# Kernel tuning notes

Hardware: AMD Instinct MI355X
Metric: run time of the kernel (lower is better)

## Reference

```python
import jax, jax.numpy as jnp
import numpy as np

B, T, C, H, D = 8, 1, 4096, 32, 128
P, PS = 32, 128  # num pages, page size


def setup_inputs() -> dict:
    key = jax.random.key(0)
    ks = jax.random.split(key, 8)
    w = 0.02  # weight init scale
    return {
        "x": jax.random.normal(ks[0], (B, T, C), jnp.float32),
        "k_pages": jax.random.normal(ks[1], (P, B, H, PS, D), jnp.float32),
        "v_pages": jax.random.normal(ks[2], (P, B, H, PS, D), jnp.float32),
        "Wq": jax.random.normal(ks[3], (C, C), jnp.float32) * w,
        "bq": jnp.zeros((C,), jnp.float32),
        "Wk": jax.random.normal(ks[4], (C, C), jnp.float32) * w,
        "bk": jnp.zeros((C,), jnp.float32),
        "Wv": jax.random.normal(ks[5], (C, C), jnp.float32) * w,
        "bv": jnp.zeros((C,), jnp.float32),
        "Wo": jax.random.normal(ks[6], (C, C), jnp.float32) * w,
        "bo": jnp.zeros((C,), jnp.float32),
        "cur_pos": 4095,  # tokens already in cache before this step
    }


def reference(x, k_pages, v_pages, Wq, bq, Wk, bk, Wv, bv, Wo, bo, cur_pos):
    b, t, c = x.shape
    scale = 1.0 / float(np.sqrt(D))

    def proj(W, bias):
        # [B,T,C] -> [B,H,T,D]
        y = x @ W.T + bias
        return y.reshape(b, t, H, D).transpose(0, 2, 1, 3)

    q = proj(Wq, bq)
    k_new = proj(Wk, bk)
    v_new = proj(Wv, bv)

    # kv_cache.update(k, v): write the T new tokens at cur_pos (static int)
    page, off = cur_pos // PS, cur_pos % PS
    k_pages = k_pages.at[page, :, :, off:off + t, :].set(k_new)
    v_pages = v_pages.at[page, :, :, off:off + t, :].set(v_new)

    # After update cur_pos + T == P*PS, so every page is fully valid.
    # Online-softmax over pages == exact softmax over the concatenated cache.
    k_all = k_pages.transpose(1, 2, 0, 3, 4).reshape(b, H, P * PS, D)
    v_all = v_pages.transpose(1, 2, 0, 3, 4).reshape(b, H, P * PS, D)

    scores = jnp.einsum("bhtd,bhsd->bhts", q, k_all) * scale
    attn = jax.nn.softmax(scores, axis=-1)
    out = jnp.einsum("bhts,bhsd->bhtd", attn, v_all)
    out = out.transpose(0, 2, 1, 3).reshape(b, t, c)
    return out @ Wo.T + bo
```

## Files before the change

kernel.cpp:

```cpp
#include <hip/hip_runtime.h>
#include <math.h>

#define Bn 8
#define Hn 32
#define Dn 128
#define Cn 4096
#define PSn 128
#define NCHUNK 16
#define CHUNK 256

extern "C" __global__ __launch_bounds__(256) void gemv8(
    const float* __restrict__ xin,
    const float* __restrict__ W0, const float* __restrict__ b0,
    const float* __restrict__ W1, const float* __restrict__ b1,
    const float* __restrict__ W2, const float* __restrict__ b2,
    float* __restrict__ ybase)
{
    const int m    = blockIdx.y;
    const float* W    = (m == 0) ? W0 : ((m == 1) ? W1 : W2);
    const float* bias = (m == 0) ? b0 : ((m == 1) ? b1 : b2);
    float* y = ybase + (size_t)m * (Bn * Cn);

    const int wv   = threadIdx.x >> 6;
    const int lane = threadIdx.x & 63;
    const int obase = blockIdx.x * 8;

    float acc[8][8];
#pragma unroll
    for (int r = 0; r < 8; ++r)
#pragma unroll
        for (int j = 0; j < 8; ++j) acc[r][j] = 0.f;

    const float* wp = W + (size_t)obase * Cn;
#pragma unroll
    for (int it = 0; it < 4; ++it) {
        const int c = wv * 1024 + it * 256 + lane * 4;
        float4 w4[8], x4[8];
#pragma unroll
        for (int j = 0; j < 8; ++j) w4[j] = *(const float4*)(wp + (size_t)j * Cn + c);
#pragma unroll
        for (int r = 0; r < 8; ++r) x4[r] = *(const float4*)(xin + (size_t)r * Cn + c);
#pragma unroll
        for (int r = 0; r < 8; ++r)
#pragma unroll
            for (int j = 0; j < 8; ++j) {
                acc[r][j] = fmaf(x4[r].x, w4[j].x,
                            fmaf(x4[r].y, w4[j].y,
                            fmaf(x4[r].z, w4[j].z,
                            fmaf(x4[r].w, w4[j].w, acc[r][j]))));
            }
    }

    const int lr = lane >> 3, lj = lane & 7;
    float mine = 0.f;
#pragma unroll
    for (int r = 0; r < 8; ++r)
#pragma unroll
        for (int j = 0; j < 8; ++j) {
            float v = acc[r][j];
#pragma unroll
            for (int off = 32; off; off >>= 1) v += __shfl_xor(v, off);
            if (lr == r && lj == j) mine = v;
        }

    __shared__ float red[4][64];
    red[wv][lane] = mine;
    __syncthreads();
    if (threadIdx.x < 64) {
        const float s = red[0][lane] + red[1][lane] + red[2][lane] + red[3][lane]
                      + bias[obase + lj];
        y[(size_t)lr * Cn + obase + lj] = s;
    }
}

extern "C" __global__ __launch_bounds__(256) void attn_partial(
    const float* __restrict__ kp, const float* __restrict__ vp,
    const float* __restrict__ qn, const float* __restrict__ kn,
    const float* __restrict__ vn, const int* __restrict__ curp,
    float* __restrict__ pout, float* __restrict__ pml)
{
    const int chunk = blockIdx.x, h = blockIdx.y, b = blockIdx.z;
    const int tid = threadIdx.x;
    const int cur = *curp;

    __shared__ float  sc[CHUNK];
    __shared__ float  wred[8];
    __shared__ float4 red[8][32];

    const int l32 = tid & 31;
    const int g   = tid >> 5;
    const float4 q4   = *(const float4*)(qn + (size_t)b * Cn + h * Dn + l32 * 4);
    const float* newk = kn + (size_t)b * Cn + h * Dn;
    const float* newv = vn + (size_t)b * Cn + h * Dn;
    const int s0 = chunk * CHUNK;
    const float* kbase = kp + (((size_t)b * Hn + h) * PSn) * (size_t)Dn;
    const float* vbase = vp + (((size_t)b * Hn + h) * PSn) * (size_t)Dn;
    const size_t pgstride = (size_t)Bn * Hn * PSn * Dn;
    const bool has_cur = (cur >= s0) && (cur < s0 + CHUNK);

    if (!has_cur) {
#pragma unroll 8
        for (int it = 0; it < CHUNK / 8; ++it) {
            const int sl = it * 8 + g;
            const int s  = s0 + sl;
            const float* krow = kbase + (size_t)(s >> 7) * pgstride + (size_t)(s & 127) * Dn;
            const float4 k4 = *(const float4*)(krow + l32 * 4);
            float d = fmaf(q4.x,k4.x, fmaf(q4.y,k4.y, fmaf(q4.z,k4.z, q4.w*k4.w)));
#pragma unroll
            for (int off = 16; off; off >>= 1) d += __shfl_xor(d, off);
            if (l32 == 0) sc[sl] = d * 0.08838834764831845f;
        }
    } else {
#pragma unroll 4
        for (int it = 0; it < CHUNK / 8; ++it) {
            const int sl = it * 8 + g;
            const int s  = s0 + sl;
            const float* krow = (s == cur) ? newk
                : kbase + (size_t)(s >> 7) * pgstride + (size_t)(s & 127) * Dn;
            const float4 k4 = *(const float4*)(krow + l32 * 4);
            float d = fmaf(q4.x,k4.x, fmaf(q4.y,k4.y, fmaf(q4.z,k4.z, q4.w*k4.w)));
#pragma unroll
            for (int off = 16; off; off >>= 1) d += __shfl_xor(d, off);
            if (l32 == 0) sc[sl] = d * 0.08838834764831845f;
        }
    }
    __syncthreads();

    float m = sc[tid];
#pragma unroll
    for (int off = 32; off; off >>= 1) m = fmaxf(m, __shfl_xor(m, off));
    if ((tid & 63) == 0) wred[tid >> 6] = m;
    __syncthreads();
    m = fmaxf(fmaxf(wred[0], wred[1]), fmaxf(wred[2], wred[3]));
    const float p = __expf(sc[tid] - m);
    sc[tid] = p;
    float l = p;
#pragma unroll
    for (int off = 32; off; off >>= 1) l += __shfl_xor(l, off);
    if ((tid & 63) == 0) wred[4 + (tid >> 6)] = l;
    __syncthreads();
    const float lsum = wred[4] + wred[5] + wred[6] + wred[7];

    const int d4 = tid & 31;
    const int sg = tid >> 5;
    float4 acc = make_float4(0.f, 0.f, 0.f, 0.f);
    if (!has_cur) {
#pragma unroll 4
        for (int it = 0; it < 32; ++it) {
            const int sl = it * 8 + sg;
            const int s  = s0 + sl;
            const float* vrow = vbase + (size_t)(s >> 7) * pgstride + (size_t)(s & 127) * Dn;
            const float4 v4 = *(const float4*)(vrow + d4 * 4);
            const float pw = sc[sl];
            acc.x = fmaf(pw, v4.x, acc.x);
            acc.y = fmaf(pw, v4.y, acc.y);
            acc.z = fmaf(pw, v4.z, acc.z);
            acc.w = fmaf(pw, v4.w, acc.w);
        }
    } else {
#pragma unroll 2
        for (int it = 0; it < 32; ++it) {
            const int sl = it * 8 + sg;
            const int s  = s0 + sl;
            const float* vrow = (s == cur) ? newv
                : vbase + (size_t)(s >> 7) * pgstride + (size_t)(s & 127) * Dn;
            const float4 v4 = *(const float4*)(vrow + d4 * 4);
            const float pw = sc[sl];
            acc.x = fmaf(pw, v4.x, acc.x);
            acc.y = fmaf(pw, v4.y, acc.y);
            acc.z = fmaf(pw, v4.z, acc.z);
            acc.w = fmaf(pw, v4.w, acc.w);
        }
    }
    red[sg][d4] = acc;
    __syncthreads();
    const int head = b * Hn + h;
    if (tid < 32) {
        float4 o = make_float4(0.f, 0.f, 0.f, 0.f);
#pragma unroll
        for (int i = 0; i < 8; ++i) {
            const float4 t = red[i][tid];
            o.x += t.x; o.y += t.y; o.z += t.z; o.w += t.w;
        }
        float* dst = pout + ((size_t)(head * NCHUNK + chunk)) * Dn + tid * 4;
        *(float4*)dst = o;
    }
    if (tid == 0) {
        pml[(head * NCHUNK + chunk) * 2 + 0] = m;
        pml[(head * NCHUNK + chunk) * 2 + 1] = lsum;
    }
}

extern "C" __global__ __launch_bounds__(128) void attn_combine(
    const float* __restrict__ pout, const float* __restrict__ pml,
    float* __restrict__ aout)
{
    const int head = blockIdx.x;
    const int tid  = threadIdx.x;
    __shared__ float ml[NCHUNK * 2];
    if (tid < NCHUNK * 2) ml[tid] = pml[head * NCHUNK * 2 + tid];
    __syncthreads();
    float mstar = -1e30f;
#pragma unroll
    for (int i = 0; i < NCHUNK; ++i) mstar = fmaxf(mstar, ml[2 * i]);
    float L = 0.f, acc = 0.f;
#pragma unroll
    for (int i = 0; i < NCHUNK; ++i) {
        const float w = __expf(ml[2 * i] - mstar);
        L   += ml[2 * i + 1] * w;
        acc += w * pout[((size_t)head * NCHUNK + i) * Dn + tid];
    }
    aout[(size_t)head * Dn + tid] = acc / L;
}

extern "C" void kernel_launch(void* const* d_in, const int* in_sizes, int n_in,
                              void* d_out, int out_size, void* d_ws, size_t ws_size,
                              hipStream_t stream)
{
    const float* x  = (const float*)d_in[0];
    const float* kp = (const float*)d_in[1];
    const float* vp = (const float*)d_in[2];
    const float* Wq = (const float*)d_in[3];
    const float* bq = (const float*)d_in[4];
    const float* Wk = (const float*)d_in[5];
    const float* bk = (const float*)d_in[6];
    const float* Wv = (const float*)d_in[7];
    const float* bv = (const float*)d_in[8];
    const float* Wo = (const float*)d_in[9];
    const float* bo = (const float*)d_in[10];
    const int* curp = (const int*)d_in[11];

    float* ws   = (float*)d_ws;
    float* q    = ws;
    float* kn   = ws + 32768;
    float* vn   = ws + 65536;
    float* pout = ws + 98304;
    float* pml  = ws + 622592;
    float* aout = ws + 630784;
    float* dout = (float*)d_out;

    gemv8<<<dim3(512, 3), 256, 0, stream>>>(x, Wq, bq, Wk, bk, Wv, bv, q);
    attn_partial<<<dim3(NCHUNK, Hn, Bn), 256, 0, stream>>>(kp, vp, q, kn, vn, curp, pout, pml);
    attn_combine<<<256, 128, 0, stream>>>(pout, pml, aout);
    gemv8<<<dim3(512, 1), 256, 0, stream>>>(aout, Wo, bo, Wo, bo, Wo, bo, dout);
}
```

Before: 271.1 us.

## Replace two-pass chunked attention with per-wave online-softmax flash decoding

After: 314.5 us. +16.0%, slower.

```diff
diff --git a/kernel.cpp b/kernel.cpp
--- a/kernel.cpp
+++ b/kernel.cpp
@@ -6,8 +6,8 @@
 #define Dn 128
 #define Cn 4096
 #define PSn 128
-#define NCHUNK 16
-#define CHUNK 256
+#define NCHUNK 32
+#define CHUNK 128
 
 extern "C" __global__ __launch_bounds__(256) void gemv8(
     const float* __restrict__ xin,
@@ -73,121 +73,95 @@
     }
 }
 
-extern "C" __global__ __launch_bounds__(256) void attn_partial(
+extern "C" __global__ __launch_bounds__(256) void attn_flash(
     const float* __restrict__ kp, const float* __restrict__ vp,
     const float* __restrict__ qn, const float* __restrict__ kn,
     const float* __restrict__ vn, const int* __restrict__ curp,
     float* __restrict__ pout, float* __restrict__ pml)
 {
-    const int chunk = blockIdx.x, h = blockIdx.y, b = blockIdx.z;
-    const int tid = threadIdx.x;
+    const int wv    = threadIdx.x >> 6;
+    const int lane  = threadIdx.x & 63;
+    const int l32   = lane & 31;
+    const int sg    = lane >> 5;
+    const int chunk = blockIdx.x * 4 + wv;
+    const int h = blockIdx.y, b = blockIdx.z;
     const int cur = *curp;
 
-    __shared__ float  sc[CHUNK];
-    __shared__ float  wred[8];
-    __shared__ float4 red[8][32];
-
-    const int l32 = tid & 31;
-    const int g   = tid >> 5;
-    const float4 q4   = *(const float4*)(qn + (size_t)b * Cn + h * Dn + l32 * 4);
+    const float4 q4 = *(const float4*)(qn + (size_t)b * Cn + h * Dn + l32 * 4);
+    const size_t pgstride = (size_t)Bn * Hn * PSn * Dn;
+    const size_t slice    = (((size_t)b * Hn + h) * PSn) * (size_t)Dn;
+    const float* kpg  = kp + (size_t)chunk * pgstride + slice;
+    const float* vpg  = vp + (size_t)chunk * pgstride + slice;
     const float* newk = kn + (size_t)b * Cn + h * Dn;
     const float* newv = vn + (size_t)b * Cn + h * Dn;
-    const int s0 = chunk * CHUNK;
-    const float* kbase = kp + (((size_t)b * Hn + h) * PSn) * (size_t)Dn;
-    const float* vbase = vp + (((size_t)b * Hn + h) * PSn) * (size_t)Dn;
-    const size_t pgstride = (size_t)Bn * Hn * PSn * Dn;
-    const bool has_cur = (cur >= s0) && (cur < s0 + CHUNK);
-
-    if (!has_cur) {
-#pragma unroll 8
-        for (int it = 0; it < CHUNK / 8; ++it) {
-            const int sl = it * 8 + g;
-            const int s  = s0 + sl;
-            const float* krow = kbase + (size_t)(s >> 7) * pgstride + (size_t)(s & 127) * Dn;
-            const float4 k4 = *(const float4*)(krow + l32 * 4);
-            float d = fmaf(q4.x,k4.x, fmaf(q4.y,k4.y, fmaf(q4.z,k4.z, q4.w*k4.w)));
-#pragma unroll
-            for (int off = 16; off; off >>= 1) d += __shfl_xor(d, off);
-            if (l32 == 0) sc[sl] = d * 0.08838834764831845f;
-        }
-    } else {
-#pragma unroll 4
-        for (int it = 0; it < CHUNK / 8; ++it) {
-            const int sl = it * 8 + g;
-            const int s  = s0 + sl;
-            const float* krow = (s == cur) ? newk
-                : kbase + (size_t)(s >> 7) * pgstride + (size_t)(s & 127) * Dn;
-            const float4 k4 = *(const float4*)(krow + l32 * 4);
-            float d = fmaf(q4.x,k4.x, fmaf(q4.y,k4.y, fmaf(q4.z,k4.z, q4.w*k4.w)));
-#pragma unroll
-            for (int off = 16; off; off >>= 1) d += __shfl_xor(d, off);
-            if (l32 == 0) sc[sl] = d * 0.08838834764831845f;
-        }
-    }
-    __syncthreads();
-
-    float m = sc[tid];
-#pragma unroll
-    for (int off = 32; off; off >>= 1) m = fmaxf(m, __shfl_xor(m, off));
-    if ((tid & 63) == 0) wred[tid >> 6] = m;
-    __syncthreads();
-    m = fmaxf(fmaxf(wred[0], wred[1]), fmaxf(wred[2], wred[3]));
-    const float p = __expf(sc[tid] - m);
-    sc[tid] = p;
-    float l = p;
-#pragma unroll
-    for (int off = 32; off; off >>= 1) l += __shfl_xor(l, off);
-    if ((tid & 63) == 0) wred[4 + (tid >> 6)] = l;
-    __syncthreads();
-    const float lsum = wred[4] + wred[5] + wred[6] + wred[7];
-
-    const int d4 = tid & 31;
-    const int sg = tid >> 5;
+    const bool has_cur = ((cur >> 7) == chunk);
+    const float scale = 0.08838834764831845f;
+
+    float m = -1e30f, l = 0.f;
     float4 acc = make_float4(0.f, 0.f, 0.f, 0.f);
+
     if (!has_cur) {
 #pragma unroll 4
-        for (int it = 0; it < 32; ++it) {
-            const int sl = it * 8 + sg;
-            const int s  = s0 + sl;
-            const float* vrow = vbase + (size_t)(s >> 7) * pgstride + (size_t)(s & 127) * Dn;
-            const float4 v4 = *(const float4*)(vrow + d4 * 4);
-            const float pw = sc[sl];
-            acc.x = fmaf(pw, v4.x, acc.x);
-            acc.y = fmaf(pw, v4.y, acc.y);
-            acc.z = fmaf(pw, v4.z, acc.z);
-            acc.w = fmaf(pw, v4.w, acc.w);
+        for (int it = 0; it < 64; ++it) {
+            const int r = it * 2 + sg;
+            const float4 k4 = *(const float4*)(kpg + (size_t)r * Dn + l32 * 4);
+            const float4 v4 = *(const float4*)(vpg + (size_t)r * Dn + l32 * 4);
+            float d = fmaf(k4.x,q4.x, fmaf(k4.y,q4.y, fmaf(k4.z,q4.z, k4.w*q4.w)));
+#pragma unroll
+            for (int off = 16; off; off >>= 1) d += __shfl_xor(d, off);
+            const float s  = d * scale;
+            const float mn = fmaxf(m, s);
+            const float c  = __expf(m - mn);
+            const float p  = __expf(s - mn);
+            l = fmaf(l, c, p);
+            acc.x = fmaf(acc.x, c, p * v4.x);
+            acc.y = fmaf(acc.y, c, p * v4.y);
+            acc.z = fmaf(acc.z, c, p * v4.z);
+            acc.w = fmaf(acc.w, c, p * v4.w);
+            m = mn;
         }
     } else {
 #pragma unroll 2
-        for (int it = 0; it < 32; ++it) {
-            const int sl = it * 8 + sg;
-            const int s  = s0 + sl;
-            const float* vrow = (s == cur) ? newv
-                : vbase + (size_t)(s >> 7) * pgstride + (size_t)(s & 127) * Dn;
-            const float4 v4 = *(const float4*)(vrow + d4 * 4);
-            const float pw = sc[sl];
-            acc.x = fmaf(pw, v4.x, acc.x);
-            acc.y = fmaf(pw, v4.y, acc.y);
-            acc.z = fmaf(pw, v4.z, acc.z);
-            acc.w = fmaf(pw, v4.w, acc.w);
-        }
-    }
-    red[sg][d4] = acc;
-    __syncthreads();
+        for (int it = 0; it < 64; ++it) {
+            const int r = it * 2 + sg;
+            const int s_glob = chunk * CHUNK + r;
+            const float* krow = (s_glob == cur) ? newk : (kpg + (size_t)r * Dn);
+            const float* vrow = (s_glob == cur) ? newv : (vpg + (size_t)r * Dn);
+            const float4 k4 = *(const float4*)(krow + l32 * 4);
+            const float4 v4 = *(const float4*)(vrow + l32 * 4);
+            float d = fmaf(k4.x,q4.x, fmaf(k4.y,q4.y, fmaf(k4.z,q4.z, k4.w*q4.w)));
+#pragma unroll
+            for (int off = 16; off; off >>= 1) d += __shfl_xor(d, off);
+            const float s  = d * scale;
+            const float mn = fmaxf(m, s);
+            const float c  = __expf(m - mn);
+            const float p  = __expf(s - mn);
+            l = fmaf(l, c, p);
+            acc.x = fmaf(acc.x, c, p * v4.x);
+            acc.y = fmaf(acc.y, c, p * v4.y);
+            acc.z = fmaf(acc.z, c, p * v4.z);
+            acc.w = fmaf(acc.w, c, p * v4.w);
+            m = mn;
+        }
+    }
+
+    const float mo = __shfl_xor(m, 32);
+    const float mn = fmaxf(m, mo);
+    const float c  = __expf(m - mn);
+    l *= c; acc.x *= c; acc.y *= c; acc.z *= c; acc.w *= c;
+    l     += __shfl_xor(l, 32);
+    acc.x += __shfl_xor(acc.x, 32);
+    acc.y += __shfl_xor(acc.y, 32);
+    acc.z += __shfl_xor(acc.z, 32);
+    acc.w += __shfl_xor(acc.w, 32);
+
     const int head = b * Hn + h;
-    if (tid < 32) {
-        float4 o = make_float4(0.f, 0.f, 0.f, 0.f);
-#pragma unroll
-        for (int i = 0; i < 8; ++i) {
-            const float4 t = red[i][tid];
-            o.x += t.x; o.y += t.y; o.z += t.z; o.w += t.w;
-        }
-        float* dst = pout + ((size_t)(head * NCHUNK + chunk)) * Dn + tid * 4;
-        *(float4*)dst = o;
-    }
-    if (tid == 0) {
-        pml[(head * NCHUNK + chunk) * 2 + 0] = m;
-        pml[(head * NCHUNK + chunk) * 2 + 1] = lsum;
+    if (sg == 0) {
+        *(float4*)(pout + ((size_t)head * NCHUNK + chunk) * Dn + l32 * 4) = acc;
+        if (l32 == 0) {
+            pml[(head * NCHUNK + chunk) * 2 + 0] = mn;
+            pml[(head * NCHUNK + chunk) * 2 + 1] = l;
+        }
     }
 }
 
@@ -204,7 +178,7 @@
 #pragma unroll
     for (int i = 0; i < NCHUNK; ++i) mstar = fmaxf(mstar, ml[2 * i]);
     float L = 0.f, acc = 0.f;
-#pragma unroll
+#pragma unroll 8
     for (int i = 0; i < NCHUNK; ++i) {
         const float w = __expf(ml[2 * i] - mstar);
         L   += ml[2 * i + 1] * w;
@@ -235,12 +209,12 @@
     float* kn   = ws + 32768;
     float* vn   = ws + 65536;
     float* pout = ws + 98304;
-    float* pml  = ws + 622592;
-    float* aout = ws + 630784;
+    float* pml  = ws + 1146880;
+    float* aout = ws + 1163264;
     float* dout = (float*)d_out;
 
     gemv8<<<dim3(512, 3), 256, 0, stream>>>(x, Wq, bq, Wk, bk, Wv, bv, q);
-    attn_partial<<<dim3(NCHUNK, Hn, Bn), 256, 0, stream>>>(kp, vp, q, kn, vn, curp, pout, pml);
+    attn_flash<<<dim3(NCHUNK / 4, Hn, Bn), 256, 0, stream>>>(kp, vp, q, kn, vn, curp, pout, pml);
     attn_combine<<<256, 128, 0, stream>>>(pout, pml, aout);
     gemv8<<<dim3(512, 1), 256, 0, stream>>>(aout, Wo, bo, Wo, bo, Wo, bo, dout);
 }
```
